# Kernel optimization log

Measured on AMD Instinct MI355X. Metric: run time of the kernel, lower is better.

Reference implementation:

```python
import jax, jax.numpy as jnp
import numpy as np

B, T, H, V = 32, 128, 1024, 32000


def setup_inputs() -> dict:
    key = jax.random.key(0)
    ks = jax.random.split(key, 10)
    s = 0.02
    return {
        "y_input": jax.random.normal(ks[0], (B, T), dtype=jnp.float32),
        "encoder_hidden_states": jax.random.normal(ks[1], (B, H), dtype=jnp.float32),
        "W_h": jax.random.normal(ks[2], (H, H), dtype=jnp.float32) * s,   # h_projection (no bias)
        "W_c": jax.random.normal(ks[3], (H, H), dtype=jnp.float32) * s,   # c_projection (no bias)
        "W_ih": jax.random.normal(ks[4], (4 * H, 1 + H), dtype=jnp.float32) * s,
        "W_hh": jax.random.normal(ks[5], (4 * H, H), dtype=jnp.float32) * s,
        "b_ih": jax.random.normal(ks[6], (4 * H,), dtype=jnp.float32) * s,
        "b_hh": jax.random.normal(ks[7], (4 * H,), dtype=jnp.float32) * s,
        "W_out": jax.random.normal(ks[8], (V, H), dtype=jnp.float32) * s,
        "b_out": jax.random.normal(ks[9], (V,), dtype=jnp.float32) * s,
    }


def reference(y_input, encoder_hidden_states, W_h, W_c, W_ih, W_hh, b_ih, b_hh, W_out, b_out):
    # init hidden/cell from encoder states (bias-free projections)
    h0 = encoder_hidden_states @ W_h.T  # [B, H]
    c0 = encoder_hidden_states @ W_c.T  # [B, H]

    def step(carry, x_t):
        h, c = carry
        ybar = jnp.concatenate([x_t[:, None], h], axis=-1)           # [B, 1+H]
        gates = ybar @ W_ih.T + b_ih + h @ W_hh.T + b_hh             # [B, 4H]
        i, f, g, o = jnp.split(gates, 4, axis=-1)                    # torch LSTMCell gate order
        i = jax.nn.sigmoid(i)
        f = jax.nn.sigmoid(f)
        g = jnp.tanh(g)
        o = jax.nn.sigmoid(o)
        c_new = f * c + i * g
        h_new = o * jnp.tanh(c_new)
        return (h_new, c_new), h_new

    _, hs = jax.lax.scan(step, (h0, c0), y_input.T)  # hs: [T, B, H]
    logits = hs @ W_out.T + b_out                    # [T, B, V]
    return jnp.transpose(logits, (1, 2, 0))          # [B, V, T]
```

## Files before the change

kernel.cpp:

```cpp
#include <hip/hip_runtime.h>
#include <hip/hip_bf16.h>
#include <stdint.h>

#define B_ 32
#define T_ 128
#define H_ 1024
#define V_ 32000
#define NBLK_REC 64

typedef unsigned short u16;
typedef __attribute__((ext_vector_type(8))) short short8;
typedef __attribute__((ext_vector_type(4))) float f32x4;

static __device__ __forceinline__ u16 f2bf(float f) {
    uint32_t u = __float_as_uint(f);
    uint32_t r = (u + 0x7FFFu + ((u >> 16) & 1u)) >> 16;
    return (u16)r;
}

static __device__ __forceinline__ float sigmf(float x) {
    return 1.0f / (1.0f + __expf(-x));
}

static __device__ __forceinline__ float tanh_f(float x) {
    x = fminf(fmaxf(x, -20.f), 20.f);
    float e = __expf(2.f * x);
    return (e - 1.f) / (e + 1.f);
}

static __device__ __forceinline__ void gload16(const void* g, void* l) {
    __builtin_amdgcn_global_load_lds(
        (const __attribute__((address_space(1))) uint32_t*)g,
        (__attribute__((address_space(3))) uint32_t*)(uint32_t)(uintptr_t)l,
        16, 0, 0);
}

__global__ void prep_w(const float* __restrict__ Wih, const float* __restrict__ Whh,
                       const float* __restrict__ bih, const float* __restrict__ bhh,
                       u16* __restrict__ Wc, float* __restrict__ wx, float* __restrict__ biasc,
                       unsigned* __restrict__ flags) {
    int idx = blockIdx.x * 256 + threadIdx.x;
    int r = idx >> 10, k = idx & 1023;
    float v = Wih[r * (H_ + 1) + 1 + k] + Whh[idx];
    Wc[idx] = f2bf(v);
    if (k == 0) {
        wx[r] = Wih[r * (H_ + 1)];
        biasc[r] = bih[r] + bhh[r];
    }
    if (idx < 2048) flags[idx] = 0u;
}

__global__ void prep_wout(const float* __restrict__ Wout, u16* __restrict__ Wo) {
    long long i = (long long)(blockIdx.x) * 256 + threadIdx.x;
    f32x4 v = *(const f32x4*)(Wout + i * 4);
    uint2 o;
    o.x = (uint32_t)f2bf(v[0]) | ((uint32_t)f2bf(v[1]) << 16);
    o.y = (uint32_t)f2bf(v[2]) | ((uint32_t)f2bf(v[3]) << 16);
    *(uint2*)(Wo + i * 4) = o;
}

__global__ void init_hc(const float* __restrict__ enc, const float* __restrict__ Wh,
                        const float* __restrict__ Wcp, u16* __restrict__ h0,
                        float* __restrict__ c0) {
    int gwid = blockIdx.x * 4 + (threadIdx.x >> 6);
    int lane = threadIdx.x & 63;
    int sel = gwid >> 10;
    int j = gwid & 1023;
    const float* W = sel ? Wcp : Wh;
    const float* wrow = W + (size_t)j * H_;
    f32x4 wv[4];
#pragma unroll
    for (int it = 0; it < 4; ++it)
        wv[it] = *(const f32x4*)(wrow + it * 256 + lane * 4);
#pragma unroll 2
    for (int b = 0; b < B_; ++b) {
        const float* erow = enc + (size_t)b * H_;
        float acc = 0.f;
#pragma unroll
        for (int it = 0; it < 4; ++it) {
            f32x4 ev = *(const f32x4*)(erow + it * 256 + lane * 4);
            acc += wv[it][0] * ev[0] + wv[it][1] * ev[1] + wv[it][2] * ev[2] + wv[it][3] * ev[3];
        }
#pragma unroll
        for (int s = 32; s >= 1; s >>= 1) acc += __shfl_xor(acc, s, 64);
        if (lane == 0) {
            if (sel) c0[(size_t)b * H_ + j] = acc;
            else     h0[(size_t)b * H_ + j] = f2bf(acc);
        }
    }
}

__global__ __launch_bounds__(512, 2) void fused_all(
    const u16* __restrict__ Wc, const float* __restrict__ wx,
    const float* __restrict__ biasc, const u16* __restrict__ h0,
    const float* __restrict__ c0, const float* __restrict__ y,
    u16* __restrict__ A, unsigned* __restrict__ flags,
    const u16* __restrict__ Wo, const float* __restrict__ bout,
    float* __restrict__ out) {
    __shared__ __align__(16) u16 sb[65536];

    int tid = threadIdx.x;
    int lane = tid & 63;

    if (blockIdx.x < NBLK_REC) {
        float* red = (float*)sb;
        float* cs  = red + 8 * 2112;
        float* wxs = cs + 16 * 33;
        float* bcs = wxs + 64;
        float* ys  = bcs + 64;

        int kw = tid >> 6;
        int bid = blockIdx.x;
        int j0 = bid * 16;
        int jl = lane & 15;
        int kc = (lane >> 4) * 8;
        int jlx = tid & 15, pb = tid >> 4;

        short8 afr[4][4];
        {
            const u16* abase = Wc + (size_t)(j0 + jl) * H_ + kw * 128 + kc;
#pragma unroll
            for (int g = 0; g < 4; ++g)
#pragma unroll
                for (int ks = 0; ks < 4; ++ks)
                    afr[g][ks] = *(const short8*)(abase + (size_t)g * H_ * H_ + ks * 32);
        }
#pragma unroll
        for (int g = 0; g < 4; ++g)
#pragma unroll
            for (int ks = 0; ks < 4; ++ks)
                asm volatile("" : "+v"(afr[g][ks]));

        if (tid < 64) {
            int g = tid >> 4, qq = tid & 15;
            wxs[tid] = wx[(size_t)g * H_ + j0 + qq];
            bcs[tid] = biasc[(size_t)g * H_ + j0 + qq];
        }
#pragma unroll
        for (int i = tid; i < B_ * T_; i += 512)
            ys[(i >> 7) * 129 + (i & 127)] = y[i];
        cs[jlx * 33 + pb] = c0[(size_t)pb * H_ + j0 + jlx];
        __syncthreads();

        for (int t = 0; t < T_; ++t) {
            const u16* hp = (t == 0) ? h0 : (A + (size_t)(t - 1) * B_ * H_);

            if (t > 0) {
                const unsigned* fp = &flags[(kw * 8 + (lane & 7)) * 32];
                unsigned target = (unsigned)t;
                int guard = 0;
                for (;;) {
                    unsigned v = __hip_atomic_load(fp, __ATOMIC_RELAXED, __HIP_MEMORY_SCOPE_AGENT);
                    if (__all(v >= target)) break;
                    if (++guard > 20000000) break;
                }
                __atomic_signal_fence(__ATOMIC_ACQUIRE);
            }

            short8 bf0[4], bf1[4];
            {
                const u16* hb = hp + (size_t)jl * H_ + kw * 128 + kc;
#pragma unroll
                for (int ks = 0; ks < 4; ++ks) {
                    bf0[ks] = *(const short8*)(hb + ks * 32);
                    bf1[ks] = *(const short8*)(hb + (size_t)16 * H_ + ks * 32);
                }
            }
            f32x4 acc[4][2] = {};
#pragma unroll
            for (int ks = 0; ks < 4; ++ks) {
#pragma unroll
                for (int g = 0; g < 4; ++g) {
                    acc[g][0] = __builtin_amdgcn_mfma_f32_16x16x32_bf16(afr[g][ks], bf0[ks], acc[g][0], 0, 0, 0);
                    acc[g][1] = __builtin_amdgcn_mfma_f32_16x16x32_bf16(afr[g][ks], bf1[ks], acc[g][1], 0, 0, 0);
                }
            }
            int r0 = (lane >> 4) * 4;
#pragma unroll
            for (int g = 0; g < 4; ++g)
#pragma unroll
                for (int bt = 0; bt < 2; ++bt)
#pragma unroll
                    for (int r = 0; r < 4; ++r)
                        red[kw * 2112 + (g * 16 + r0 + r) * 33 + bt * 16 + jl] = acc[g][bt][r];
            __syncthreads();

            {
                float yv = ys[pb * 129 + t];
                float pg[4];
#pragma unroll
                for (int g = 0; g < 4; ++g) {
                    int row = (g * 16 + jlx) * 33 + pb;
                    float sum = red[row];
#pragma unroll
                    for (int ww = 1; ww < 8; ++ww) sum += red[ww * 2112 + row];
                    pg[g] = sum + wxs[g * 16 + jlx] * yv + bcs[g * 16 + jlx];
                }
                float iv = sigmf(pg[0]);
                float fv = sigmf(pg[1]);
                float gv = tanh_f(pg[2]);
                float ov = sigmf(pg[3]);
                float cv = fv * cs[jlx * 33 + pb] + iv * gv;
                cs[jlx * 33 + pb] = cv;
                float hv = ov * tanh_f(cv);

                unsigned h16 = (unsigned)f2bf(hv);
                unsigned oth = (unsigned)__shfl((int)h16, lane + 1, 64);
                if (!(jlx & 1)) {
                    uint32_t pk = h16 | (oth << 16);
                    __hip_atomic_store((uint32_t*)(A + ((size_t)t * B_ + pb) * H_ + j0 + jlx),
                                       pk, __ATOMIC_RELAXED, __HIP_MEMORY_SCOPE_AGENT);
                }
            }
            __syncthreads();
            if (tid == 0)
                __hip_atomic_store(&flags[bid * 32], (unsigned)(t + 1),
                                   __ATOMIC_RELAXED, __HIP_MEMORY_SCOPE_AGENT);
        }
        return;
    }

    int orig = blockIdx.x - NBLK_REC;
    int tb = orig / 500;
    int wp = orig - tb * 500;
    int xcd = wp & 7, rest = wp >> 3;
    int wg = (xcd < 4 ? xcd * 63 : 252 + (xcd - 4) * 62) + rest;
    int bb = wg / 125;
    int nb = wg - bb * 125;
    int n0g = nb << 8;

    int wid = tid >> 6;
    int wm = wid >> 2, wn = wid & 3;
    int jl = lane & 15, kq = lane >> 4;

    f32x4 acc[8][4] = {};

    auto stage = [&](int tile, int h) {
        u16* dst = sb + ((tile & 1) << 15) + (h << 13) + tid * 8;
#pragma unroll
        for (int ld = 0; ld < 2; ++ld) {
            int p = tid + (ld << 9);
            int row = p >> 3;
            int c16 = (p & 7) ^ (row & 7);
            const u16* src;
            if (h < 2)
                src = A + ((size_t)(tb * 32 + (row & 31)) * B_
                           + (size_t)(bb * 8 + h * 4 + (row >> 5))) * H_
                        + tile * 64 + c16 * 8;
            else
                src = Wo + (size_t)(n0g + ((h - 2) << 7) + row) * H_
                         + tile * 64 + c16 * 8;
            gload16(src, dst + (ld << 12));
        }
    };

    stage(0, 2); stage(0, 3);

    if (wid == 0) {
        unsigned target = (unsigned)((tb + 1) * 32);
        const unsigned* fp = &flags[lane * 32];
        int guard = 0;
        for (;;) {
            unsigned v = __hip_atomic_load(fp, __ATOMIC_RELAXED, __HIP_MEMORY_SCOPE_AGENT);
            if (__all(v >= target)) break;
            __builtin_amdgcn_s_sleep(32);
            if (++guard > 20000000) break;
        }
        __atomic_signal_fence(__ATOMIC_ACQUIRE);
    }
    __builtin_amdgcn_s_barrier();

    stage(0, 0); stage(0, 1); stage(1, 0); stage(1, 2);
    asm volatile("s_waitcnt vmcnt(4)" ::: "memory");
    __builtin_amdgcn_s_barrier();

    const int NT = 16;
    for (int tile = 0; tile < NT; ++tile) {
        const u16* buf = sb + ((tile & 1) << 15);
#pragma unroll
        for (int q = 0; q < 4; ++q) {
            const int mh = q >> 1, nh = q & 1;
            short8 af[4][2], bfr[2][2];
            const u16* bufA = buf + (mh << 13);
            const u16* bufB = buf + (1 << 14) + (nh << 13);
#pragma unroll
            for (int i = 0; i < 4; ++i) {
                int row = wm * 64 + (i << 4) + jl;
                int rx = (row & 7) << 3;
#pragma unroll
                for (int k2 = 0; k2 < 2; ++k2)
                    af[i][k2] = *(const short8*)(bufA + row * 64 + (((k2 << 5) + (kq << 3)) ^ rx));
            }
#pragma unroll
            for (int i = 0; i < 2; ++i) {
                int row = wn * 32 + (i << 4) + jl;
                int rx = (row & 7) << 3;
#pragma unroll
                for (int k2 = 0; k2 < 2; ++k2)
                    bfr[i][k2] = *(const short8*)(bufB + row * 64 + (((k2 << 5) + (kq << 3)) ^ rx));
            }
            if (q == 0) { if (tile + 1 < NT) stage(tile + 1, 1); }
            if (q == 1) { if (tile + 1 < NT) stage(tile + 1, 3); }
            if (q == 2) { if (tile + 2 < NT) stage(tile + 2, 0); }
            if (q == 3) { if (tile + 2 < NT) stage(tile + 2, 2); }

            asm volatile("" ::: "memory");
            __builtin_amdgcn_s_barrier();
            asm volatile("" ::: "memory");
            __builtin_amdgcn_s_setprio(1);
#pragma unroll
            for (int i = 0; i < 4; ++i)
#pragma unroll
                for (int jn = 0; jn < 2; ++jn)
#pragma unroll
                    for (int k2 = 0; k2 < 2; ++k2)
                        acc[mh * 4 + i][nh * 2 + jn] =
                            __builtin_amdgcn_mfma_f32_16x16x32_bf16(
                                af[i][k2], bfr[jn][k2], acc[mh * 4 + i][nh * 2 + jn], 0, 0, 0);
            __builtin_amdgcn_s_setprio(0);
            if (q == 3) {
                if (tile < 14) asm volatile("s_waitcnt vmcnt(4)" ::: "memory");
                else           asm volatile("s_waitcnt vmcnt(0)" ::: "memory");
            }
            asm volatile("" ::: "memory");
            __builtin_amdgcn_s_barrier();
        }
    }

    __syncthreads();
    float* wsl = (float*)sb + wid * 2048;
#pragma unroll
    for (int nt = 0; nt < 4; ++nt) {
        {
            int n = n0g + ((nt >> 1) << 7) + wn * 32 + ((nt & 1) << 4) + jl;
            float bias = bout[n];
#pragma unroll
            for (int mt = 0; mt < 8; ++mt) {
                int mh = mt >> 2, i = mt & 3;
                int b2 = mh * 2 + (i >> 1);
                int g = ((i & 1) << 2) + kq;
                f32x4 v = acc[mt][nt];
                v[0] += bias; v[1] += bias; v[2] += bias; v[3] += bias;
                *(f32x4*)(wsl + jl * 128 + b2 * 32 + ((g ^ (jl & 7)) << 2)) = v;
            }
        }
#pragma unroll
        for (int rr = 0; rr < 2; ++rr) {
            int flat = lane * 2 + rr;
            int jr = flat >> 3;
            int b2r = (flat >> 1) & 3;
            int h2 = flat & 1;
            int n2 = n0g + ((nt >> 1) << 7) + wn * 32 + ((nt & 1) << 4) + jr;
            int bo = bb * 8 + (b2r >> 1) * 4 + wm * 2 + (b2r & 1);
            int t0 = tb * 32 + h2 * 16;
            float* dst = out + ((size_t)bo * V_ + n2) * T_ + t0;
            const float* sp = wsl + jr * 128 + b2r * 32;
#pragma unroll
            for (int gg = 0; gg < 4; ++gg) {
                int g2 = h2 * 4 + gg;
                f32x4 v = *(const f32x4*)(sp + ((g2 ^ (jr & 7)) << 2));
                *(f32x4*)(dst + (gg << 2)) = v;
            }
        }
    }
}

extern "C" void kernel_launch(void* const* d_in, const int* in_sizes, int n_in,
                              void* d_out, int out_size, void* d_ws, size_t ws_size,
                              hipStream_t stream) {
    const float* y    = (const float*)d_in[0];
    const float* enc  = (const float*)d_in[1];
    const float* Wh   = (const float*)d_in[2];
    const float* Wcp  = (const float*)d_in[3];
    const float* Wih  = (const float*)d_in[4];
    const float* Whh  = (const float*)d_in[5];
    const float* bih  = (const float*)d_in[6];
    const float* bhh  = (const float*)d_in[7];
    const float* Wout = (const float*)d_in[8];
    const float* bout = (const float*)d_in[9];

    uint8_t* ws = (uint8_t*)d_ws;
    u16*  Wcomb = (u16*)ws;
    u16*  Wo    = (u16*)(ws + 8388608);
    float* wx    = (float*)(ws + 8388608 + 65536000);
    float* biasc = wx + 4096;
    u16*  h0    = (u16*)(biasc + 4096);
    float* c     = (float*)(h0 + 32 * 1024);
    u16*  A     = (u16*)(c + 32 * 1024);
    unsigned* flags = (unsigned*)(A + (size_t)4096 * 1024);

    prep_w<<<16384, 256, 0, stream>>>(Wih, Whh, bih, bhh, Wcomb, wx, biasc, flags);
    prep_wout<<<32000, 256, 0, stream>>>(Wout, Wo);
    init_hc<<<512, 256, 0, stream>>>(enc, Wh, Wcp, h0, c);

    fused_all<<<NBLK_REC + 2000, 512, 0, stream>>>(
        Wcomb, wx, biasc, h0, c, y, A, flags, Wo, bout, (float*)d_out);
}
```

Baseline: 740.6 us.

## Use per-wave flags for recurrence sync and retile output GEMM to 16 timesteps

Recurrent blocks now publish a per-wave progress flag right after each wave writes its slice of h, and consumer waves poll the specific per-wave flags they depend on instead of per-block flags set after a block-wide barrier. The output projection is retiled so each workgroup covers 16 timesteps by 16 batch rows rather than 32 by 8, which lets it start after every 16 steps instead of 32 and overlap more with the recurrence. The LDS transpose epilogue is replaced by direct 16-byte global stores of the accumulators. The cost is more flag memory and polling traffic, plus a store pattern that writes only 64 contiguous bytes per row.

```diff
diff --git a/kernel.cpp b/kernel.cpp
--- a/kernel.cpp
+++ b/kernel.cpp
@@ -47,7 +47,7 @@
         wx[r] = Wih[r * (H_ + 1)];
         biasc[r] = bih[r] + bhh[r];
     }
-    if (idx < 2048) flags[idx] = 0u;
+    if (idx < 18432) flags[idx] = 0u;
 }
 
 __global__ void prep_wout(const float* __restrict__ Wout, u16* __restrict__ Wo) {
@@ -146,7 +146,7 @@
             const u16* hp = (t == 0) ? h0 : (A + (size_t)(t - 1) * B_ * H_);
 
             if (t > 0) {
-                const unsigned* fp = &flags[(kw * 8 + (lane & 7)) * 32];
+                const unsigned* fp = &flags[2048 + (((kw << 6) + lane) << 5)];
                 unsigned target = (unsigned)t;
                 int guard = 0;
                 for (;;) {
@@ -211,6 +211,11 @@
                     __hip_atomic_store((uint32_t*)(A + ((size_t)t * B_ + pb) * H_ + j0 + jlx),
                                        pk, __ATOMIC_RELAXED, __HIP_MEMORY_SCOPE_AGENT);
                 }
+                asm volatile("s_waitcnt vmcnt(0)" ::: "memory");
+                if (lane == 0)
+                    __hip_atomic_store(&flags[2048 + (((bid << 3) + kw) << 5)],
+                                       (unsigned)(t + 1),
+                                       __ATOMIC_RELAXED, __HIP_MEMORY_SCOPE_AGENT);
             }
             __syncthreads();
             if (tid == 0)
@@ -221,10 +226,10 @@
     }
 
     int orig = blockIdx.x - NBLK_REC;
-    int tb = orig / 500;
-    int wp = orig - tb * 500;
+    int tb = orig / 250;
+    int wp = orig - tb * 250;
     int xcd = wp & 7, rest = wp >> 3;
-    int wg = (xcd < 4 ? xcd * 63 : 252 + (xcd - 4) * 62) + rest;
+    int wg = (xcd < 2 ? xcd * 32 : 64 + (xcd - 2) * 31) + rest;
     int bb = wg / 125;
     int nb = wg - bb * 125;
     int n0g = nb << 8;
@@ -244,8 +249,8 @@
             int c16 = (p & 7) ^ (row & 7);
             const u16* src;
             if (h < 2)
-                src = A + ((size_t)(tb * 32 + (row & 31)) * B_
-                           + (size_t)(bb * 8 + h * 4 + (row >> 5))) * H_
+                src = A + ((size_t)(tb * 16 + (row & 15)) * B_
+                           + (size_t)(bb * 16 + h * 8 + (row >> 4))) * H_
                         + tile * 64 + c16 * 8;
             else
                 src = Wo + (size_t)(n0g + ((h - 2) << 7) + row) * H_
@@ -257,7 +262,7 @@
     stage(0, 2); stage(0, 3);
 
     if (wid == 0) {
-        unsigned target = (unsigned)((tb + 1) * 32);
+        unsigned target = (unsigned)((tb + 1) * 16);
         const unsigned* fp = &flags[lane * 32];
         int guard = 0;
         for (;;) {
@@ -327,40 +332,17 @@
         }
     }
 
-    __syncthreads();
-    float* wsl = (float*)sb + wid * 2048;
 #pragma unroll
     for (int nt = 0; nt < 4; ++nt) {
-        {
-            int n = n0g + ((nt >> 1) << 7) + wn * 32 + ((nt & 1) << 4) + jl;
-            float bias = bout[n];
-#pragma unroll
-            for (int mt = 0; mt < 8; ++mt) {
-                int mh = mt >> 2, i = mt & 3;
-                int b2 = mh * 2 + (i >> 1);
-                int g = ((i & 1) << 2) + kq;
-                f32x4 v = acc[mt][nt];
-                v[0] += bias; v[1] += bias; v[2] += bias; v[3] += bias;
-                *(f32x4*)(wsl + jl * 128 + b2 * 32 + ((g ^ (jl & 7)) << 2)) = v;
-            }
-        }
-#pragma unroll
-        for (int rr = 0; rr < 2; ++rr) {
-            int flat = lane * 2 + rr;
-            int jr = flat >> 3;
-            int b2r = (flat >> 1) & 3;
-            int h2 = flat & 1;
-            int n2 = n0g + ((nt >> 1) << 7) + wn * 32 + ((nt & 1) << 4) + jr;
-            int bo = bb * 8 + (b2r >> 1) * 4 + wm * 2 + (b2r & 1);
-            int t0 = tb * 32 + h2 * 16;
-            float* dst = out + ((size_t)bo * V_ + n2) * T_ + t0;
-            const float* sp = wsl + jr * 128 + b2r * 32;
-#pragma unroll
-            for (int gg = 0; gg < 4; ++gg) {
-                int g2 = h2 * 4 + gg;
-                f32x4 v = *(const f32x4*)(sp + ((g2 ^ (jr & 7)) << 2));
-                *(f32x4*)(dst + (gg << 2)) = v;
-            }
+        int n = n0g + ((nt >> 1) << 7) + wn * 32 + ((nt & 1) << 4) + jl;
+        float bias = bout[n];
+#pragma unroll
+        for (int mt = 0; mt < 8; ++mt) {
+            int bo = bb * 16 + ((mt >> 2) << 3) + wm * 4 + (mt & 3);
+            f32x4 v = acc[mt][nt];
+            v[0] += bias; v[1] += bias; v[2] += bias; v[3] += bias;
+            float* dst = out + ((size_t)bo * V_ + n) * T_ + tb * 16 + (kq << 2);
+            *(f32x4*)dst = v;
         }
     }
 }
```

Result: slower. 796.3 us (+7.5%).
